# Performance work log

Measured on AMD Instinct MI355X. Metric: run time of the kernel, lower is better.

## Reference

```python
import jax, jax.numpy as jnp
import numpy as np

NUM_HEADS = 16
HEAD_DIM = 64


def setup_inputs() -> dict:
    key = jax.random.key(0)
    k1, k2, k3 = jax.random.split(key, 3)
    B, N, D = 4, 2048, NUM_HEADS * HEAD_DIM
    q = jax.random.normal(k1, (B, N, D), dtype=jnp.float32)
    k = jax.random.normal(k2, (B, N, D), dtype=jnp.float32)
    v = jax.random.normal(k3, (B, N, D), dtype=jnp.float32)
    # causal mask: True where attention is allowed
    attn_mask = jnp.tril(jnp.ones((N, N), dtype=bool))
    return {"q": q, "k": k, "v": v, "attn_mask": attn_mask}


def reference(q, k, v, attn_mask):
    B, N, D = q.shape
    H, Hd = NUM_HEADS, HEAD_DIM
    # [B, N, H*Hd] -> [B, H, N, Hd]
    qh = q.reshape(B, N, H, Hd).transpose(0, 2, 1, 3)
    kh = k.reshape(B, N, H, Hd).transpose(0, 2, 1, 3)
    vh = v.reshape(B, N, H, Hd).transpose(0, 2, 1, 3)
    scale = 1.0 / jnp.sqrt(jnp.asarray(Hd, dtype=q.dtype))
    scores = jnp.einsum('bhqd,bhkd->bhqk', qh, kh) * scale  # [B,H,N,N]
    scores = jnp.where(attn_mask[None, None, :, :], scores, -jnp.inf)
    probs = jax.nn.softmax(scores, axis=-1)
    y = jnp.einsum('bhqk,bhkd->bhqd', probs, vh)  # [B,H,N,Hd]
    return y.transpose(0, 2, 1, 3).reshape(B, N, H * Hd)
```

## Files before the change

kernel.cpp:

```cpp
#include <hip/hip_runtime.h>

#define RS 1024
#define SEQLEN 2048

typedef __fp16 f16;
typedef __attribute__((ext_vector_type(2))) __fp16 half2v;
typedef __attribute__((ext_vector_type(4))) __fp16 half4v;
typedef __attribute__((ext_vector_type(8))) __fp16 half8v;
typedef __attribute__((ext_vector_type(4))) float float4v;

__device__ __forceinline__ half8v pack8h(float4v a, float4v b) {
  union { half8v v; half2v h[4]; } u;
  u.h[0] = __builtin_amdgcn_cvt_pkrtz(a[0], a[1]);
  u.h[1] = __builtin_amdgcn_cvt_pkrtz(a[2], a[3]);
  u.h[2] = __builtin_amdgcn_cvt_pkrtz(b[0], b[1]);
  u.h[3] = __builtin_amdgcn_cvt_pkrtz(b[2], b[3]);
  return u.v;
}

template<bool DOMASK>
__device__ __forceinline__ void compute_tile(
    const f16* __restrict__ Klds, const f16* __restrict__ VB,
    const half8v (&aq)[2][2], float4v (&o)[2][4], float (&lp)[2],
    int quad, int lm, int wlm0)
{
  #pragma unroll
  for (int h = 0; h < 2; ++h) {
    float4v sfr[2][2];
    #pragma unroll
    for (int a = 0; a < 2; ++a)
      #pragma unroll
      for (int nn = 0; nn < 2; ++nn) sfr[a][nn] = (float4v){0.f, 0.f, 0.f, 0.f};

    __builtin_amdgcn_s_setprio(1);
    #pragma unroll
    for (int nn = 0; nn < 2; ++nn) {
      const int row = (2*h + nn)*16 + lm;
      #pragma unroll
      for (int s = 0; s < 2; ++s) {
        const half8v ak = *(const half8v*)&Klds[row*64 + (((s*4 + quad) ^ (lm & 7)) * 8)];
        sfr[0][nn] = __builtin_amdgcn_mfma_f32_16x16x32_f16(ak, aq[0][s], sfr[0][nn], 0, 0, 0);
        sfr[1][nn] = __builtin_amdgcn_mfma_f32_16x16x32_f16(ak, aq[1][s], sfr[1][nn], 0, 0, 0);
      }
    }
    __builtin_amdgcn_s_setprio(0);

    half4v pa[2][2];
    #pragma unroll
    for (int a = 0; a < 2; ++a) {
      const int wlm = wlm0 + a*16;
      float acc = 0.f;
      #pragma unroll
      for (int nn = 0; nn < 2; ++nn) {
        const int nb = 2*h + nn;
        float p[4];
        #pragma unroll
        for (int r = 0; r < 4; ++r) {
          const int n = nb*16 + quad*4 + r;
          const float e = __builtin_amdgcn_exp2f(sfr[a][nn][r]);
          p[r] = (DOMASK && (n > wlm)) ? 0.f : e;
        }
        acc += (p[0] + p[1]) + (p[2] + p[3]);
        union { half4v v; half2v h2[2]; } u;
        u.h2[0] = __builtin_amdgcn_cvt_pkrtz(p[0], p[1]);
        u.h2[1] = __builtin_amdgcn_cvt_pkrtz(p[2], p[3]);
        pa[a][nn] = u.v;
      }
      lp[a] += acc;
    }

    __builtin_amdgcn_s_setprio(1);
    #pragma unroll
    for (int e = 0; e < 2; ++e) {
      #pragma unroll
      for (int nn = 0; nn < 2; ++nn) {
        const int kvq = (2*h + nn)*4 + quad;
        union { half8v v; half4v hh[2]; } uu;
        uu.v = *(const half8v*)&VB[kvq*256 + (((e*16 + lm) ^ kvq) * 8)];
        o[0][2*e]     = __builtin_amdgcn_mfma_f32_16x16x16f16(pa[0][nn], uu.hh[0], o[0][2*e],     0, 0, 0);
        o[0][2*e + 1] = __builtin_amdgcn_mfma_f32_16x16x16f16(pa[0][nn], uu.hh[1], o[0][2*e + 1], 0, 0, 0);
        o[1][2*e]     = __builtin_amdgcn_mfma_f32_16x16x16f16(pa[1][nn], uu.hh[0], o[1][2*e],     0, 0, 0);
        o[1][2*e + 1] = __builtin_amdgcn_mfma_f32_16x16x16f16(pa[1][nn], uu.hh[1], o[1][2*e + 1], 0, 0, 0);
      }
    }
    __builtin_amdgcn_s_setprio(0);
  }
}

__global__ __launch_bounds__(256, 3) void fa_fwd(
    const float* __restrict__ Qg, const float* __restrict__ Kg,
    const float* __restrict__ Vg, float* __restrict__ Og)
{
  __shared__ __align__(16) f16 Klds[2][64*64];
  __shared__ __align__(16) f16 VB[2][64*64];

  const int tid  = threadIdx.x;
  const int w    = tid >> 6;
  const int lane = tid & 63;
  const int quad = lane >> 4;
  const int lm   = lane & 15;
  const int wlm0 = (w & 1)*32 + lm;

  const int bid = blockIdx.x;
  const int bh  = bid & 63;
  const int g   = (bid >> 6) & 3;
  const int s   = bid >> 8;
  const int st  = (s == 0) ? 15 - g : (s == 1) ? 8 + g : (s == 2) ? 7 - g : g;
  const int j1  = 2*st + 1;
  const int j1w = 2*st + (w >> 1);

  const size_t headoff = (size_t)(bh >> 4) * SEQLEN * RS + (size_t)(bh & 15) * 64;
  const float* Kb = Kg + headoff;
  const float* Vb = Vg + headoff;

  const float qs = 0.18033688011112042f;
  half8v aq[2][2];
  #pragma unroll
  for (int a = 0; a < 2; ++a) {
    const float* qp = Qg + headoff + (size_t)(st*128 + w*32 + a*16 + lm) * RS + quad*8;
    aq[a][0] = pack8h(*(const float4v*)qp * qs,        *(const float4v*)(qp + 4) * qs);
    aq[a][1] = pack8h(*(const float4v*)(qp + 32) * qs, *(const float4v*)(qp + 36) * qs);
  }

  float4v o[2][4] = {};
  float lp[2] = {0.f, 0.f};

  const int krow = tid >> 3, kcb = tid & 7;
  const int rgrp = tid >> 4, dgrp = tid & 15;
  const int ve   = dgrp >> 3;
  const int vv   = (dgrp >> 2) & 1;
  const int lmb  = (dgrp & 3) * 4;

  auto stageKtile = [&](int kv0, f16* Kd) {
    const float* kp = Kb + (size_t)(kv0 + krow) * RS + kcb*8;
    const float4v k0 = *(const float4v*)kp;
    const float4v k1 = *(const float4v*)(kp + 4);
    const float* kp2 = kp + (size_t)32 * RS;
    const float4v k2 = *(const float4v*)kp2;
    const float4v k3 = *(const float4v*)(kp2 + 4);
    *(half8v*)&Kd[krow*64 + ((kcb ^ (krow & 7)) * 8)] = pack8h(k0, k1);
    const int row2 = krow + 32;
    *(half8v*)&Kd[row2*64 + ((kcb ^ (row2 & 7)) * 8)] = pack8h(k2, k3);
  };
  auto stageVtile = [&](int kv0, f16* Vd) {
    const float* vp = Vb + (size_t)(kv0 + rgrp*4) * RS + dgrp*4;
    const float4v v0 = *(const float4v*)vp;
    const float4v v1 = *(const float4v*)(vp + RS);
    const float4v v2 = *(const float4v*)(vp + 2*RS);
    const float4v v3 = *(const float4v*)(vp + 3*RS);
    #pragma unroll
    for (int cc = 0; cc < 4; ++cc) {
      union { half4v v; half2v h[2]; } u;
      u.h[0] = __builtin_amdgcn_cvt_pkrtz(v0[cc], v1[cc]);
      u.h[1] = __builtin_amdgcn_cvt_pkrtz(v2[cc], v3[cc]);
      const int lmv = lmb + cc;
      *(half4v*)&Vd[rgrp*256 + (((ve*16 + lmv) ^ rgrp) * 8) + vv*4] = u.v;
    }
  };

  stageKtile(0, Klds[0]);
  stageVtile(0, VB[0]);
  __syncthreads();

  for (int j = 0; j <= j1; ++j) {
    const int cur = j & 1;
    if (j < j1) {
      stageKtile((j + 1) * 64, Klds[cur ^ 1]);
      stageVtile((j + 1) * 64, VB[cur ^ 1]);
    }
    if (j <= j1w) {
      if (j < j1w)
        compute_tile<false>(Klds[cur], VB[cur], aq, o, lp, quad, lm, wlm0);
      else
        compute_tile<true >(Klds[cur], VB[cur], aq, o, lp, quad, lm, wlm0);
    }
    __syncthreads();
  }

  #pragma unroll
  for (int a = 0; a < 2; ++a) {
    float l = lp[a];
    l += __shfl_xor(l, 16);
    l += __shfl_xor(l, 32);
    const float linv = 1.0f / l;
    #pragma unroll
    for (int r = 0; r < 4; ++r) {
      const float nrm = __shfl(linv, quad*4 + r);
      float* op = Og + headoff + (size_t)(st*128 + w*32 + a*16 + quad*4 + r) * RS;
      #pragma unroll
      for (int db = 0; db < 4; ++db)
        op[db*16 + lm] = o[a][db][r] * nrm;
    }
  }
}

extern "C" void kernel_launch(void* const* d_in, const int* in_sizes, int n_in,
                              void* d_out, int out_size, void* d_ws, size_t ws_size,
                              hipStream_t stream) {
  const float* q = (const float*)d_in[0];
  const float* k = (const float*)d_in[1];
  const float* v = (const float*)d_in[2];
  float* out = (float*)d_out;
  fa_fwd<<<dim3(16 * 64), dim3(256), 0, stream>>>(q, k, v, out);
}
```

Measured before the change: 193.7 us.

## Single-buffer K/V, keep Q in LDS, and raise occupancy to 4 blocks

Drops the K/V double buffer, so each iteration computes on the current tile, syncs, then stages the next tile and syncs again. Q fragments move from registers into LDS and are re-read once per tile. The V LDS swizzle is also changed to cut bank conflicts. The aim is to free registers and LDS so launch bounds can rise from 3 to 4 blocks per CU, at the cost of losing load/compute overlap within a block and adding a second barrier per tile.

```diff
diff --git a/kernel.cpp b/kernel.cpp
--- a/kernel.cpp
+++ b/kernel.cpp
@@ -21,9 +21,17 @@
 template<bool DOMASK>
 __device__ __forceinline__ void compute_tile(
     const f16* __restrict__ Klds, const f16* __restrict__ VB,
-    const half8v (&aq)[2][2], float4v (&o)[2][4], float (&lp)[2],
-    int quad, int lm, int wlm0)
+    const f16* __restrict__ Qlds, float4v (&o)[2][4], float (&lp)[2],
+    int tid, int quad, int lm, int wlm0)
 {
+  const int plm = lm ^ (lm >> 3);
+  half8v aqr[2][2];
+  #pragma unroll
+  for (int a = 0; a < 2; ++a)
+    #pragma unroll
+    for (int s = 0; s < 2; ++s)
+      aqr[a][s] = *(const half8v*)&Qlds[((a*2 + s)*256 + tid)*8];
+
   #pragma unroll
   for (int h = 0; h < 2; ++h) {
     float4v sfr[2][2];
@@ -39,8 +47,8 @@
       #pragma unroll
       for (int s = 0; s < 2; ++s) {
         const half8v ak = *(const half8v*)&Klds[row*64 + (((s*4 + quad) ^ (lm & 7)) * 8)];
-        sfr[0][nn] = __builtin_amdgcn_mfma_f32_16x16x32_f16(ak, aq[0][s], sfr[0][nn], 0, 0, 0);
-        sfr[1][nn] = __builtin_amdgcn_mfma_f32_16x16x32_f16(ak, aq[1][s], sfr[1][nn], 0, 0, 0);
+        sfr[0][nn] = __builtin_amdgcn_mfma_f32_16x16x32_f16(ak, aqr[0][s], sfr[0][nn], 0, 0, 0);
+        sfr[1][nn] = __builtin_amdgcn_mfma_f32_16x16x32_f16(ak, aqr[1][s], sfr[1][nn], 0, 0, 0);
       }
     }
     __builtin_amdgcn_s_setprio(0);
@@ -76,7 +84,7 @@
       for (int nn = 0; nn < 2; ++nn) {
         const int kvq = (2*h + nn)*4 + quad;
         union { half8v v; half4v hh[2]; } uu;
-        uu.v = *(const half8v*)&VB[kvq*256 + (((e*16 + lm) ^ kvq) * 8)];
+        uu.v = *(const half8v*)&VB[kvq*256 + (((e*16 + plm) ^ kvq) * 8)];
         o[0][2*e]     = __builtin_amdgcn_mfma_f32_16x16x16f16(pa[0][nn], uu.hh[0], o[0][2*e],     0, 0, 0);
         o[0][2*e + 1] = __builtin_amdgcn_mfma_f32_16x16x16f16(pa[0][nn], uu.hh[1], o[0][2*e + 1], 0, 0, 0);
         o[1][2*e]     = __builtin_amdgcn_mfma_f32_16x16x16f16(pa[1][nn], uu.hh[0], o[1][2*e],     0, 0, 0);
@@ -87,12 +95,13 @@
   }
 }
 
-__global__ __launch_bounds__(256, 3) void fa_fwd(
+__global__ __launch_bounds__(256, 4) void fa_fwd(
     const float* __restrict__ Qg, const float* __restrict__ Kg,
     const float* __restrict__ Vg, float* __restrict__ Og)
 {
-  __shared__ __align__(16) f16 Klds[2][64*64];
-  __shared__ __align__(16) f16 VB[2][64*64];
+  __shared__ __align__(16) f16 Klds[64*64];
+  __shared__ __align__(16) f16 VB[64*64];
+  __shared__ __align__(16) f16 Qlds[4*256*8];
 
   const int tid  = threadIdx.x;
   const int w    = tid >> 6;
@@ -114,12 +123,13 @@
   const float* Vb = Vg + headoff;
 
   const float qs = 0.18033688011112042f;
-  half8v aq[2][2];
   #pragma unroll
   for (int a = 0; a < 2; ++a) {
     const float* qp = Qg + headoff + (size_t)(st*128 + w*32 + a*16 + lm) * RS + quad*8;
-    aq[a][0] = pack8h(*(const float4v*)qp * qs,        *(const float4v*)(qp + 4) * qs);
-    aq[a][1] = pack8h(*(const float4v*)(qp + 32) * qs, *(const float4v*)(qp + 36) * qs);
+    const half8v q0 = pack8h(*(const float4v*)qp * qs,        *(const float4v*)(qp + 4) * qs);
+    const half8v q1 = pack8h(*(const float4v*)(qp + 32) * qs, *(const float4v*)(qp + 36) * qs);
+    *(half8v*)&Qlds[((a*2 + 0)*256 + tid)*8] = q0;
+    *(half8v*)&Qlds[((a*2 + 1)*256 + tid)*8] = q1;
   }
 
   float4v o[2][4] = {};
@@ -129,20 +139,20 @@
   const int rgrp = tid >> 4, dgrp = tid & 15;
   const int ve   = dgrp >> 3;
   const int vv   = (dgrp >> 2) & 1;
-  const int lmb  = (dgrp & 3) * 4;
-
-  auto stageKtile = [&](int kv0, f16* Kd) {
+  const int d3   = dgrp & 3;
+
+  auto stageKtile = [&](int kv0) {
     const float* kp = Kb + (size_t)(kv0 + krow) * RS + kcb*8;
     const float4v k0 = *(const float4v*)kp;
     const float4v k1 = *(const float4v*)(kp + 4);
     const float* kp2 = kp + (size_t)32 * RS;
     const float4v k2 = *(const float4v*)kp2;
     const float4v k3 = *(const float4v*)(kp2 + 4);
-    *(half8v*)&Kd[krow*64 + ((kcb ^ (krow & 7)) * 8)] = pack8h(k0, k1);
+    *(half8v*)&Klds[krow*64 + ((kcb ^ (krow & 7)) * 8)] = pack8h(k0, k1);
     const int row2 = krow + 32;
-    *(half8v*)&Kd[row2*64 + ((kcb ^ (row2 & 7)) * 8)] = pack8h(k2, k3);
+    *(half8v*)&Klds[row2*64 + ((kcb ^ (row2 & 7)) * 8)] = pack8h(k2, k3);
   };
-  auto stageVtile = [&](int kv0, f16* Vd) {
+  auto stageVtile = [&](int kv0) {
     const float* vp = Vb + (size_t)(kv0 + rgrp*4) * RS + dgrp*4;
     const float4v v0 = *(const float4v*)vp;
     const float4v v1 = *(const float4v*)(vp + RS);
@@ -153,26 +163,26 @@
       union { half4v v; half2v h[2]; } u;
       u.h[0] = __builtin_amdgcn_cvt_pkrtz(v0[cc], v1[cc]);
       u.h[1] = __builtin_amdgcn_cvt_pkrtz(v2[cc], v3[cc]);
-      const int lmv = lmb + cc;
-      *(half4v*)&Vd[rgrp*256 + (((ve*16 + lmv) ^ rgrp) * 8) + vv*4] = u.v;
+      const int sx = (ve*16 + d3*4 + (cc ^ (d3 >> 1))) ^ rgrp;
+      *(half4v*)&VB[rgrp*256 + sx*8 + vv*4] = u.v;
     }
   };
 
-  stageKtile(0, Klds[0]);
-  stageVtile(0, VB[0]);
+  stageKtile(0);
+  stageVtile(0);
   __syncthreads();
 
   for (int j = 0; j <= j1; ++j) {
-    const int cur = j & 1;
-    if (j < j1) {
-      stageKtile((j + 1) * 64, Klds[cur ^ 1]);
-      stageVtile((j + 1) * 64, VB[cur ^ 1]);
-    }
     if (j <= j1w) {
       if (j < j1w)
-        compute_tile<false>(Klds[cur], VB[cur], aq, o, lp, quad, lm, wlm0);
+        compute_tile<false>(Klds, VB, Qlds, o, lp, tid, quad, lm, wlm0);
       else
-        compute_tile<true >(Klds[cur], VB[cur], aq, o, lp, quad, lm, wlm0);
+        compute_tile<true >(Klds, VB, Qlds, o, lp, tid, quad, lm, wlm0);
+    }
+    __syncthreads();
+    if (j < j1) {
+      stageKtile((j + 1) * 64);
+      stageVtile((j + 1) * 64);
     }
     __syncthreads();
   }
```

Result: no change. 195.1 us (+0.7%).
